# Performance work log

Measured on AMD Instinct MI355X. Metric: run time of the kernel, lower is better.

## Reference

```python
import jax, jax.numpy as jnp
import numpy as np

NODES, NFEAT = 128, 256


def setup_inputs() -> dict:
    key = jax.random.key(0)
    k1, k2, k3, k4, k5, k6 = jax.random.split(key, 6)
    B = 512
    x = jax.random.normal(k1, (B, NODES, NFEAT), dtype=jnp.float32)
    adj = jax.random.uniform(k2, (B, NODES, NODES), dtype=jnp.float32)
    # GraphConvolution(nfeat, nfeat): weight [nfeat, nfeat], bias [nfeat]
    s = 1.0 / np.sqrt(NFEAT)
    gcn_w = jax.random.uniform(k3, (NFEAT, NFEAT), minval=-s, maxval=s, dtype=jnp.float32)
    gcn_b = jax.random.uniform(k4, (NFEAT,), minval=-s, maxval=s, dtype=jnp.float32)
    # fc: Linear(nfeat*nodes, nfeat), torch layout [out, in]
    s2 = 1.0 / np.sqrt(NFEAT * NODES)
    fc_w = jax.random.uniform(k5, (NFEAT, NFEAT * NODES), minval=-s2, maxval=s2, dtype=jnp.float32)
    fc_b = jax.random.uniform(k6, (NFEAT,), minval=-s2, maxval=s2, dtype=jnp.float32)
    return {"x": x, "adj": adj, "gcn_w": gcn_w, "gcn_b": gcn_b, "fc_w": fc_w, "fc_b": fc_b}


def reference(x, adj, gcn_w, gcn_b, fc_w, fc_b):
    B = x.shape[0]
    # Per-sample loop GCN fused as batched matmuls:
    # support = X @ W ; out = A @ support + b
    support = jnp.einsum('bnf,fg->bng', x, gcn_w)          # [B, nodes, nfeat]
    mid = jnp.einsum('bnm,bmg->bng', adj, support) + gcn_b  # [B, nodes, nfeat]
    # cat along dim0 then reshape(-1, nfeat*nodes) == per-graph flatten
    flat = mid.reshape(B, NODES * NFEAT)
    output = flat @ fc_w.T + fc_b                           # [B, nfeat]
    useful_input = x[:, 0, :]                               # [B, nfeat]
    return (output, useful_input, output)
```

## Files before the change

### kernel.cpp

```cpp
#include <hip/hip_runtime.h>

#define NODES 128
#define NFEAT 256
#define BATCH 512
#define KTOT  (NODES * NFEAT)
#define SPLIT 64
#define KCH   (KTOT / SPLIT)

typedef __bf16 bf16_t;
typedef bf16_t bf16x8 __attribute__((ext_vector_type(8)));
typedef float  f32x4  __attribute__((ext_vector_type(4)));

#define BK    32
#define LDK   40
#define BK2   64
#define LDK2  72
#define LDM   136
#define TILE  128

__device__ __forceinline__ void bar() {
    asm volatile("s_waitcnt lgkmcnt(0)\n\ts_barrier" ::: "memory");
}

__device__ __forceinline__ bf16x8 cvt8(const float4 a, const float4 b) {
    bf16x8 t;
    t[0] = (bf16_t)a.x; t[1] = (bf16_t)a.y; t[2] = (bf16_t)a.z; t[3] = (bf16_t)a.w;
    t[4] = (bf16_t)b.x; t[5] = (bf16_t)b.y; t[6] = (bf16_t)b.z; t[7] = (bf16_t)b.w;
    return t;
}

struct XT { float4 v[4]; };
__device__ __forceinline__ void xload(const float* __restrict__ src, int ld, int k0,
                                      int tid, XT& t) {
#pragma unroll
    for (int i = 0; i < 2; i++) {
        int f = tid + i * 256, r = f >> 2, c = f & 3;
        t.v[2 * i]     = *(const float4*)(src + (size_t)r * ld + k0 + c * 8);
        t.v[2 * i + 1] = *(const float4*)(src + (size_t)r * ld + k0 + c * 8 + 4);
    }
}
__device__ __forceinline__ void xstore(bf16_t* __restrict__ dst, int tid, const XT& t) {
#pragma unroll
    for (int i = 0; i < 2; i++) {
        int f = tid + i * 256, r = f >> 2, c = f & 3;
        *(bf16x8*)(dst + r * LDK + c * 8) = cvt8(t.v[2 * i], t.v[2 * i + 1]);
    }
}

struct XT2 { float4 v[8]; };
__device__ __forceinline__ void xload2(const float* __restrict__ src, int ld, int k0,
                                       int tid, XT2& t) {
#pragma unroll
    for (int i = 0; i < 4; i++) {
        int f = tid + i * 256, r = f >> 3, c = f & 7;
        t.v[2 * i]     = *(const float4*)(src + (size_t)r * ld + k0 + c * 8);
        t.v[2 * i + 1] = *(const float4*)(src + (size_t)r * ld + k0 + c * 8 + 4);
    }
}
__device__ __forceinline__ void xstore2(bf16_t* __restrict__ dst, int tid, const XT2& t) {
#pragma unroll
    for (int i = 0; i < 4; i++) {
        int f = tid + i * 256, r = f >> 3, c = f & 7;
        *(bf16x8*)(dst + r * LDK2 + c * 8) = cvt8(t.v[2 * i], t.v[2 * i + 1]);
    }
}

struct AT2 { bf16x8 v[4]; };
__device__ __forceinline__ void aload2(const bf16_t* __restrict__ src, int ld, int k0,
                                       int tid, AT2& t) {
#pragma unroll
    for (int i = 0; i < 4; i++) {
        int f = tid + i * 256, r = f >> 3, c = f & 7;
        t.v[i] = *(const bf16x8*)(src + (size_t)r * ld + k0 + c * 8);
    }
}
__device__ __forceinline__ void astore2(bf16_t* __restrict__ dst, int tid, const AT2& t) {
#pragma unroll
    for (int i = 0; i < 4; i++) {
        int f = tid + i * 256, r = f >> 3, c = f & 7;
        *(bf16x8*)(dst + r * LDK2 + c * 8) = t.v[i];
    }
}

__global__ __launch_bounds__(256)
void k_wt(const float* __restrict__ w, bf16_t* __restrict__ wT) {
    const int g0 = blockIdx.x * 4;
    const int k  = threadIdx.x;
    const float4 v = *(const float4*)(w + (size_t)k * NFEAT + g0);
    wT[(size_t)(g0 + 0) * NFEAT + k] = (bf16_t)v.x;
    wT[(size_t)(g0 + 1) * NFEAT + k] = (bf16_t)v.y;
    wT[(size_t)(g0 + 2) * NFEAT + k] = (bf16_t)v.z;
    wT[(size_t)(g0 + 3) * NFEAT + k] = (bf16_t)v.w;
}

__global__ __launch_bounds__(256, 3)
void k_fused12(const float* __restrict__ x, const float* __restrict__ adj,
               const bf16_t* __restrict__ wT, const float* __restrict__ gcn_b,
               bf16_t* __restrict__ mid) {
    __shared__ __align__(16) bf16_t As[TILE * LDK];
    __shared__ __align__(16) bf16_t Sb[TILE * LDM];
    const int n0  = blockIdx.x * TILE;
    const int b   = blockIdx.y;
    const int tid = threadIdx.x;
    const int lane = tid & 63, w = tid >> 6, wm = w & 1, wn = w >> 1;
    const int l15 = lane & 15, q = lane >> 4;
    const float* xb   = x   + (size_t)b * NODES * NFEAT;
    const float* adjb = adj + (size_t)b * NODES * NODES;

    const bf16_t* wrow[4];
#pragma unroll
    for (int j = 0; j < 4; j++)
        wrow[j] = wT + (size_t)(n0 + wn * 64 + j * 16 + l15) * NFEAT + q * 8;

    f32x4 acc[4][4] = {};
    {
        XT r0, rn, r2;
        xload(xb, NFEAT, 0, tid, r0);
        xload(xb, NFEAT, BK, tid, rn);
        bf16x8 bcur[4], bnxt[4];
#pragma unroll
        for (int j = 0; j < 4; j++) bcur[j] = *(const bf16x8*)(wrow[j]);
        xstore(As, tid, r0);
        bar();
        for (int k0 = 0; k0 < NFEAT; k0 += BK) {
            const bool in1 = (k0 + BK)   < NFEAT;
            const bool in2 = (k0 + 2*BK) < NFEAT;
            if (in2) xload(xb, NFEAT, k0 + 2*BK, tid, r2);
            const int knc = in1 ? k0 + BK : 0;
#pragma unroll
            for (int j = 0; j < 4; j++) bnxt[j] = *(const bf16x8*)(wrow[j] + knc);
            bf16x8 a[4];
#pragma unroll
            for (int i = 0; i < 4; i++)
                a[i] = *(const bf16x8*)(As + (wm * 64 + i * 16 + l15) * LDK + q * 8);
#pragma unroll
            for (int i = 0; i < 4; i++)
#pragma unroll
                for (int j = 0; j < 4; j++)
                    acc[i][j] = __builtin_amdgcn_mfma_f32_16x16x32_bf16(a[i], bcur[j], acc[i][j], 0, 0, 0);
            bar();
            if (in1) xstore(As, tid, rn);
            rn = r2;
#pragma unroll
            for (int j = 0; j < 4; j++) bcur[j] = bnxt[j];
            bar();
        }
    }

    XT a0, a1, a2;
    xload(adjb, NODES, 0, tid, a0);
    xload(adjb, NODES, BK, tid, a1);
#pragma unroll
    for (int i = 0; i < 4; i++)
#pragma unroll
        for (int j = 0; j < 4; j++)
#pragma unroll
            for (int r = 0; r < 4; r++) {
                int m = wm * 64 + i * 16 + q * 4 + r;
                int g = wn * 64 + j * 16 + l15;
                Sb[g * LDM + m] = (bf16_t)acc[i][j][r];
            }
    bar();
    xstore(As, tid, a0);
    bar();

    f32x4 acc2[4][4] = {};
    for (int k0 = 0; k0 < NODES; k0 += BK) {
        const bool in1 = (k0 + BK)   < NODES;
        const bool in2 = (k0 + 2*BK) < NODES;
        if (in2) xload(adjb, NODES, k0 + 2*BK, tid, a2);
        bf16x8 a[4], bb[4];
#pragma unroll
        for (int i = 0; i < 4; i++)
            a[i] = *(const bf16x8*)(As + (wm * 64 + i * 16 + l15) * LDK + q * 8);
#pragma unroll
        for (int j = 0; j < 4; j++)
            bb[j] = *(const bf16x8*)(Sb + (wn * 64 + j * 16 + l15) * LDM + k0 + q * 8);
#pragma unroll
        for (int i = 0; i < 4; i++)
#pragma unroll
            for (int j = 0; j < 4; j++)
                acc2[i][j] = __builtin_amdgcn_mfma_f32_16x16x32_bf16(a[i], bb[j], acc2[i][j], 0, 0, 0);
        bar();
        if (in1) xstore(As, tid, a1);
        a1 = a2;
        bar();
    }
    bf16_t* outb = mid + (size_t)b * NODES * NFEAT;
#pragma unroll
    for (int j = 0; j < 4; j++) {
        int g = n0 + wn * 64 + j * 16 + l15;
        float bias = gcn_b[g];
#pragma unroll
        for (int i = 0; i < 4; i++)
#pragma unroll
            for (int r = 0; r < 4; r++) {
                int node = wm * 64 + i * 16 + q * 4 + r;
                outb[(size_t)node * NFEAT + g] = (bf16_t)(acc2[i][j][r] + bias);
            }
    }
}

__global__ __launch_bounds__(256, 3)
void k_out(const bf16_t* __restrict__ flat, const float* __restrict__ fcw,
           bf16_t* __restrict__ part) {
    __shared__ __align__(16) bf16_t As[TILE * LDK2];
    __shared__ __align__(16) bf16_t Bs[TILE * LDK2];
    const int m0 = blockIdx.x * TILE;
    const int n0 = blockIdx.y * TILE;
    const int kb = blockIdx.z * KCH, kend = kb + KCH;
    const int tid = threadIdx.x;
    const int lane = tid & 63, w = tid >> 6, wm = w & 1, wn = w >> 1;
    const int l15 = lane & 15, q = lane >> 4;
    f32x4 acc[4][4] = {};
    const bf16_t* fa = flat + (size_t)m0 * KTOT;
    const float*  fb = fcw + (size_t)n0 * KTOT;

    AT2 at; aload2(fa, KTOT, kb, tid, at);
    XT2 bt; xload2(fb, KTOT, kb, tid, bt);
    astore2(As, tid, at);
    xstore2(Bs, tid, bt);
    bar();
    for (int k0 = kb; k0 < kend; k0 += BK2) {
        const int kn = k0 + BK2;
        const bool in = kn < kend;
        AT2 an; XT2 bn;
        if (in) { aload2(fa, KTOT, kn, tid, an); xload2(fb, KTOT, kn, tid, bn); }
#pragma unroll
        for (int kk = 0; kk < BK2; kk += BK) {
            bf16x8 a[4], bbf[4];
#pragma unroll
            for (int i = 0; i < 4; i++)
                a[i] = *(const bf16x8*)(As + (wm * 64 + i * 16 + l15) * LDK2 + kk + q * 8);
#pragma unroll
            for (int j = 0; j < 4; j++)
                bbf[j] = *(const bf16x8*)(Bs + (wn * 64 + j * 16 + l15) * LDK2 + kk + q * 8);
#pragma unroll
            for (int i = 0; i < 4; i++)
#pragma unroll
                for (int j = 0; j < 4; j++)
                    acc[i][j] = __builtin_amdgcn_mfma_f32_16x16x32_bf16(a[i], bbf[j], acc[i][j], 0, 0, 0);
        }
        bar();
        if (in) { astore2(As, tid, an); xstore2(Bs, tid, bn); }
        bar();
    }
    bf16_t* pb = part + (size_t)blockIdx.z * BATCH * NFEAT;
#pragma unroll
    for (int i = 0; i < 4; i++)
#pragma unroll
        for (int j = 0; j < 4; j++)
#pragma unroll
            for (int r = 0; r < 4; r++) {
                int bt_ = m0 + wm * 64 + i * 16 + q * 4 + r;
                int o   = n0 + wn * 64 + j * 16 + l15;
                pb[(size_t)bt_ * NFEAT + o] = (bf16_t)acc[i][j][r];
            }
}

__global__ __launch_bounds__(256)
void k_reduce(const bf16_t* __restrict__ part, const float* __restrict__ fc_b,
              const float* __restrict__ x, float* __restrict__ out) {
    const int g8 = (blockIdx.x * 256 + threadIdx.x) * 8;
    const int o = g8 & (NFEAT - 1), b = g8 >> 8;
    float s[8];
    const float4 c0 = *(const float4*)(fc_b + o);
    const float4 c1 = *(const float4*)(fc_b + o + 4);
    s[0] = c0.x; s[1] = c0.y; s[2] = c0.z; s[3] = c0.w;
    s[4] = c1.x; s[5] = c1.y; s[6] = c1.z; s[7] = c1.w;
#pragma unroll 8
    for (int i = 0; i < SPLIT; i++) {
        bf16x8 p = *(const bf16x8*)(part + (size_t)i * BATCH * NFEAT + g8);
#pragma unroll
        for (int j = 0; j < 8; j++) s[j] += (float)p[j];
    }
    float4 o0 = make_float4(s[0], s[1], s[2], s[3]);
    float4 o1 = make_float4(s[4], s[5], s[6], s[7]);
    *(float4*)(out + g8)     = o0;
    *(float4*)(out + g8 + 4) = o1;
    *(float4*)(out + 2 * BATCH * NFEAT + g8)     = o0;
    *(float4*)(out + 2 * BATCH * NFEAT + g8 + 4) = o1;
    const float4 x0 = *(const float4*)(x + (size_t)b * NODES * NFEAT + o);
    const float4 x1 = *(const float4*)(x + (size_t)b * NODES * NFEAT + o + 4);
    *(float4*)(out + BATCH * NFEAT + g8)     = x0;
    *(float4*)(out + BATCH * NFEAT + g8 + 4) = x1;
}

extern "C" void kernel_launch(void* const* d_in, const int* in_sizes, int n_in,
                              void* d_out, int out_size, void* d_ws, size_t ws_size,
                              hipStream_t stream) {
    const float* x     = (const float*)d_in[0];
    const float* adj   = (const float*)d_in[1];
    const float* gcn_w = (const float*)d_in[2];
    const float* gcn_b = (const float*)d_in[3];
    const float* fc_w  = (const float*)d_in[4];
    const float* fc_b  = (const float*)d_in[5];
    float* out = (float*)d_out;

    bf16_t* wT   = (bf16_t*)d_ws;
    bf16_t* mid  = (bf16_t*)((char*)d_ws + 131072);
    bf16_t* part = (bf16_t*)((char*)d_ws + 131072 + (size_t)BATCH * NODES * NFEAT * 2);

    k_wt     <<<dim3(64), dim3(256), 0, stream>>>(gcn_w, wT);
    k_fused12<<<dim3(2, BATCH), dim3(256), 0, stream>>>(x, adj, wT, gcn_b, mid);
    k_out    <<<dim3(4, 2, SPLIT), dim3(256), 0, stream>>>(mid, fc_w, part);
    k_reduce <<<dim3(64), dim3(256), 0, stream>>>(part, fc_b, x, out);
}
```

Before: 203.7 us.

## Double-buffer LDS tiles, deepen register prefetch, swizzle support tile, widen reduce grid

Both GEMM kernels now keep two LDS stage buffers, so the next tile is stored while the current one is consumed, leaving one barrier per k-step instead of two. Register prefetch goes three tiles ahead and the k-loops are fully unrolled. The transposed support tile in LDS uses an XOR swizzle instead of padding to avoid bank conflicts. k_out drops to 2 blocks per CU for the larger LDS footprint, and k_reduce uses four elements per thread with twice as many blocks. The extra registers and LDS may lower occupancy.

```diff
diff --git a/kernel.cpp b/kernel.cpp
--- a/kernel.cpp
+++ b/kernel.cpp
@@ -8,6 +8,7 @@
 #define KCH   (KTOT / SPLIT)
 
 typedef __bf16 bf16_t;
+typedef bf16_t bf16x4 __attribute__((ext_vector_type(4)));
 typedef bf16_t bf16x8 __attribute__((ext_vector_type(8)));
 typedef float  f32x4  __attribute__((ext_vector_type(4)));
 
@@ -15,7 +16,6 @@
 #define LDK   40
 #define BK2   64
 #define LDK2  72
-#define LDM   136
 #define TILE  128
 
 __device__ __forceinline__ void bar() {
@@ -97,8 +97,8 @@
 void k_fused12(const float* __restrict__ x, const float* __restrict__ adj,
                const bf16_t* __restrict__ wT, const float* __restrict__ gcn_b,
                bf16_t* __restrict__ mid) {
-    __shared__ __align__(16) bf16_t As[TILE * LDK];
-    __shared__ __align__(16) bf16_t Sb[TILE * LDM];
+    __shared__ __align__(16) bf16_t As[2][TILE * LDK];
+    __shared__ __align__(16) bf16_t Sb[TILE * TILE];
     const int n0  = blockIdx.x * TILE;
     const int b   = blockIdx.y;
     const int tid = threadIdx.x;
@@ -114,76 +114,71 @@
 
     f32x4 acc[4][4] = {};
     {
-        XT r0, rn, r2;
-        xload(xb, NFEAT, 0, tid, r0);
-        xload(xb, NFEAT, BK, tid, rn);
-        bf16x8 bcur[4], bnxt[4];
-#pragma unroll
-        for (int j = 0; j < 4; j++) bcur[j] = *(const bf16x8*)(wrow[j]);
-        xstore(As, tid, r0);
+        XT r[3];
+        xload(xb, NFEAT, 0 * BK, tid, r[0]);
+        xload(xb, NFEAT, 1 * BK, tid, r[1]);
+        xload(xb, NFEAT, 2 * BK, tid, r[2]);
+        xstore(As[0], tid, r[0]);
         bar();
-        for (int k0 = 0; k0 < NFEAT; k0 += BK) {
-            const bool in1 = (k0 + BK)   < NFEAT;
-            const bool in2 = (k0 + 2*BK) < NFEAT;
-            if (in2) xload(xb, NFEAT, k0 + 2*BK, tid, r2);
-            const int knc = in1 ? k0 + BK : 0;
-#pragma unroll
-            for (int j = 0; j < 4; j++) bnxt[j] = *(const bf16x8*)(wrow[j] + knc);
+#pragma unroll
+        for (int k = 0; k < 8; k++) {
+            if (k + 3 < 8) xload(xb, NFEAT, (k + 3) * BK, tid, r[k % 3]);
+            bf16x8 bcur[4];
+#pragma unroll
+            for (int j = 0; j < 4; j++) bcur[j] = *(const bf16x8*)(wrow[j] + k * BK);
             bf16x8 a[4];
 #pragma unroll
             for (int i = 0; i < 4; i++)
-                a[i] = *(const bf16x8*)(As + (wm * 64 + i * 16 + l15) * LDK + q * 8);
+                a[i] = *(const bf16x8*)(&As[k & 1][(wm * 64 + i * 16 + l15) * LDK + q * 8]);
 #pragma unroll
             for (int i = 0; i < 4; i++)
 #pragma unroll
                 for (int j = 0; j < 4; j++)
                     acc[i][j] = __builtin_amdgcn_mfma_f32_16x16x32_bf16(a[i], bcur[j], acc[i][j], 0, 0, 0);
-            bar();
-            if (in1) xstore(As, tid, rn);
-            rn = r2;
-#pragma unroll
-            for (int j = 0; j < 4; j++) bcur[j] = bnxt[j];
+            if (k + 1 < 8) xstore(As[(k + 1) & 1], tid, r[(k + 1) % 3]);
             bar();
         }
     }
 
-    XT a0, a1, a2;
-    xload(adjb, NODES, 0, tid, a0);
-    xload(adjb, NODES, BK, tid, a1);
+    XT r[3];
+    xload(adjb, NODES, 0 * BK, tid, r[0]);
+    xload(adjb, NODES, 1 * BK, tid, r[1]);
+    xload(adjb, NODES, 2 * BK, tid, r[2]);
 #pragma unroll
     for (int i = 0; i < 4; i++)
 #pragma unroll
         for (int j = 0; j < 4; j++)
 #pragma unroll
-            for (int r = 0; r < 4; r++) {
-                int m = wm * 64 + i * 16 + q * 4 + r;
+            for (int rr = 0; rr < 4; rr++) {
+                int m = wm * 64 + i * 16 + q * 4 + rr;
                 int g = wn * 64 + j * 16 + l15;
-                Sb[g * LDM + m] = (bf16_t)acc[i][j][r];
+                int slot = (m >> 3) ^ (g & 15);
+                Sb[g * 128 + slot * 8 + (m & 7)] = (bf16_t)acc[i][j][rr];
             }
     bar();
-    xstore(As, tid, a0);
+    xstore(As[0], tid, r[0]);
     bar();
 
     f32x4 acc2[4][4] = {};
-    for (int k0 = 0; k0 < NODES; k0 += BK) {
-        const bool in1 = (k0 + BK)   < NODES;
-        const bool in2 = (k0 + 2*BK) < NODES;
-        if (in2) xload(adjb, NODES, k0 + 2*BK, tid, a2);
+#pragma unroll
+    for (int k = 0; k < 4; k++) {
+        if (k + 3 < 4) xload(adjb, NODES, (k + 3) * BK, tid, r[k % 3]);
         bf16x8 a[4], bb[4];
 #pragma unroll
         for (int i = 0; i < 4; i++)
-            a[i] = *(const bf16x8*)(As + (wm * 64 + i * 16 + l15) * LDK + q * 8);
-#pragma unroll
-        for (int j = 0; j < 4; j++)
-            bb[j] = *(const bf16x8*)(Sb + (wn * 64 + j * 16 + l15) * LDM + k0 + q * 8);
+            a[i] = *(const bf16x8*)(&As[k & 1][(wm * 64 + i * 16 + l15) * LDK + q * 8]);
+#pragma unroll
+        for (int j = 0; j < 4; j++) {
+            int R = wn * 64 + j * 16 + l15;
+            int slot = (k * 4 + q) ^ (R & 15);
+            bb[j] = *(const bf16x8*)(&Sb[R * 128 + slot * 8]);
+        }
 #pragma unroll
         for (int i = 0; i < 4; i++)
 #pragma unroll
             for (int j = 0; j < 4; j++)
                 acc2[i][j] = __builtin_amdgcn_mfma_f32_16x16x32_bf16(a[i], bb[j], acc2[i][j], 0, 0, 0);
-        bar();
-        if (in1) xstore(As, tid, a1);
-        a1 = a2;
+        if (k + 1 < 4) xstore(As[(k + 1) & 1], tid, r[(k + 1) % 3]);
         bar();
     }
     bf16_t* outb = mid + (size_t)b * NODES * NFEAT;
@@ -194,21 +189,21 @@
 #pragma unroll
         for (int i = 0; i < 4; i++)
 #pragma unroll
-            for (int r = 0; r < 4; r++) {
-                int node = wm * 64 + i * 16 + q * 4 + r;
-                outb[(size_t)node * NFEAT + g] = (bf16_t)(acc2[i][j][r] + bias);
+            for (int rr = 0; rr < 4; rr++) {
+                int node = wm * 64 + i * 16 + q * 4 + rr;
+                outb[(size_t)node * NFEAT + g] = (bf16_t)(acc2[i][j][rr] + bias);
             }
     }
 }
 
-__global__ __launch_bounds__(256, 3)
+__global__ __launch_bounds__(256, 2)
 void k_out(const bf16_t* __restrict__ flat, const float* __restrict__ fcw,
            bf16_t* __restrict__ part) {
-    __shared__ __align__(16) bf16_t As[TILE * LDK2];
-    __shared__ __align__(16) bf16_t Bs[TILE * LDK2];
+    __shared__ __align__(16) bf16_t As[2][TILE * LDK2];
+    __shared__ __align__(16) bf16_t Bs[2][TILE * LDK2];
     const int m0 = blockIdx.x * TILE;
     const int n0 = blockIdx.y * TILE;
-    const int kb = blockIdx.z * KCH, kend = kb + KCH;
+    const int kb = blockIdx.z * KCH;
     const int tid = threadIdx.x;
     const int lane = tid & 63, w = tid >> 6, wm = w & 1, wn = w >> 1;
     const int l15 = lane & 15, q = lane >> 4;
@@ -216,33 +211,38 @@
     const bf16_t* fa = flat + (size_t)m0 * KTOT;
     const float*  fb = fcw + (size_t)n0 * KTOT;
 
-    AT2 at; aload2(fa, KTOT, kb, tid, at);
-    XT2 bt; xload2(fb, KTOT, kb, tid, bt);
-    astore2(As, tid, at);
-    xstore2(Bs, tid, bt);
+    AT2 ra[3]; XT2 rb[2];
+    aload2(fa, KTOT, kb + 0 * BK2, tid, ra[0]);
+    xload2(fb, KTOT, kb + 0 * BK2, tid, rb[0]);
+    aload2(fa, KTOT, kb + 1 * BK2, tid, ra[1]);
+    xload2(fb, KTOT, kb + 1 * BK2, tid, rb[1]);
+    aload2(fa, KTOT, kb + 2 * BK2, tid, ra[2]);
+    astore2(As[0], tid, ra[0]);
+    xstore2(Bs[0], tid, rb[0]);
     bar();
-    for (int k0 = kb; k0 < kend; k0 += BK2) {
-        const int kn = k0 + BK2;
-        const bool in = kn < kend;
-        AT2 an; XT2 bn;
-        if (in) { aload2(fa, KTOT, kn, tid, an); xload2(fb, KTOT, kn, tid, bn); }
+#pragma unroll
+    for (int k = 0; k < 8; k++) {
+        if (k + 3 < 8) aload2(fa, KTOT, kb + (k + 3) * BK2, tid, ra[k % 3]);
+        if (k + 2 < 8) xload2(fb, KTOT, kb + (k + 2) * BK2, tid, rb[k & 1]);
 #pragma unroll
         for (int kk = 0; kk < BK2; kk += BK) {
             bf16x8 a[4], bbf[4];
 #pragma unroll
             for (int i = 0; i < 4; i++)
-                a[i] = *(const bf16x8*)(As + (wm * 64 + i * 16 + l15) * LDK2 + kk + q * 8);
+                a[i] = *(const bf16x8*)(&As[k & 1][(wm * 64 + i * 16 + l15) * LDK2 + kk + q * 8]);
 #pragma unroll
             for (int j = 0; j < 4; j++)
-                bbf[j] = *(const bf16x8*)(Bs + (wn * 64 + j * 16 + l15) * LDK2 + kk + q * 8);
+                bbf[j] = *(const bf16x8*)(&Bs[k & 1][(wn * 64 + j * 16 + l15) * LDK2 + kk + q * 8]);
 #pragma unroll
             for (int i = 0; i < 4; i++)
 #pragma unroll
                 for (int j = 0; j < 4; j++)
                     acc[i][j] = __builtin_amdgcn_mfma_f32_16x16x32_bf16(a[i], bbf[j], acc[i][j], 0, 0, 0);
         }
-        bar();
-        if (in) { astore2(As, tid, an); xstore2(Bs, tid, bn); }
+        if (k + 1 < 8) {
+            astore2(As[(k + 1) & 1], tid, ra[(k + 1) % 3]);
+            xstore2(Bs[(k + 1) & 1], tid, rb[(k + 1) & 1]);
+        }
         bar();
     }
     bf16_t* pb = part + (size_t)blockIdx.z * BATCH * NFEAT;
@@ -261,29 +261,21 @@
 __global__ __launch_bounds__(256)
 void k_reduce(const bf16_t* __restrict__ part, const float* __restrict__ fc_b,
               const float* __restrict__ x, float* __restrict__ out) {
-    const int g8 = (blockIdx.x * 256 + threadIdx.x) * 8;
-    const int o = g8 & (NFEAT - 1), b = g8 >> 8;
-    float s[8];
+    const int g4 = (blockIdx.x * 256 + threadIdx.x) * 4;
+    const int o = g4 & (NFEAT - 1), b = g4 >> 8;
+    float s[4];
     const float4 c0 = *(const float4*)(fc_b + o);
-    const float4 c1 = *(const float4*)(fc_b + o + 4);
     s[0] = c0.x; s[1] = c0.y; s[2] = c0.z; s[3] = c0.w;
-    s[4] = c1.x; s[5] = c1.y; s[6] = c1.z; s[7] = c1.w;
 #pragma unroll 8
     for (int i = 0; i < SPLIT; i++) {
-        bf16x8 p = *(const bf16x8*)(part + (size_t)i * BATCH * NFEAT + g8);
-#pragma unroll
-        for (int j = 0; j < 8; j++) s[j] += (float)p[j];
+        bf16x4 p = *(const bf16x4*)(part + (size_t)i * BATCH * NFEAT + g4);
+#pragma unroll
+        for (int j = 0; j < 4; j++) s[j] += (float)p[j];
     }
     float4 o0 = make_float4(s[0], s[1], s[2], s[3]);
-    float4 o1 = make_float4(s[4], s[5], s[6], s[7]);
-    *(float4*)(out + g8)     = o0;
-    *(float4*)(out + g8 + 4) = o1;
-    *(float4*)(out + 2 * BATCH * NFEAT + g8)     = o0;
-    *(float4*)(out + 2 * BATCH * NFEAT + g8 + 4) = o1;
-    const float4 x0 = *(const float4*)(x + (size_t)b * NODES * NFEAT + o);
-    const float4 x1 = *(const float4*)(x + (size_t)b * NODES * NFEAT + o + 4);
-    *(float4*)(out + BATCH * NFEAT + g8)     = x0;
-    *(float4*)(out + BATCH * NFEAT + g8 + 4) = x1;
+    *(float4*)(out + g4) = o0;
+    *(float4*)(out + 2 * BATCH * NFEAT + g4) = o0;
+    *(float4*)(out + BATCH * NFEAT + g4) = *(const float4*)(x + (size_t)b * NODES * NFEAT + o);
 }
 
 extern "C" void kernel_launch(void* const* d_in, const int* in_sizes, int n_in,
@@ -304,5 +296,5 @@
     k_wt     <<<dim3(64), dim3(256), 0, stream>>>(gcn_w, wT);
     k_fused12<<<dim3(2, BATCH), dim3(256), 0, stream>>>(x, adj, wT, gcn_b, mid);
     k_out    <<<dim3(4, 2, SPLIT), dim3(256), 0, stream>>>(mid, fc_w, part);
-    k_reduce <<<dim3(64), dim3(256), 0, stream>>>(part, fc_b, x, out);
-}
+    k_reduce <<<dim3(128), dim3(256), 0, stream>>>(part, fc_b, x, out);
+}
```

Measured after the change: 200.9 us. About the same (-1.4%).
